# Performance work log

Hardware: AMD Instinct MI355X
Metric: run time of the kernel (lower is better)

The kernel has to match this reference:

```python
import jax, jax.numpy as jnp
import numpy as np

N_NODES = 100000
N_EDGES = 1600000
F_IN = 512
HIDDEN = 64
N_CLASS = 16


def spmm(edge_src, edge_dst, edge_val, dense):
    # sparse [N,N] @ dense [N,D] via gather-scale-scatter
    gathered = dense[edge_src] * edge_val[:, None]          # [E, D]
    return jax.ops.segment_sum(gathered, edge_dst, num_segments=N_NODES)


def setup_inputs() -> dict:
    key = jax.random.key(0)
    ks = jax.random.split(key, 8)
    return {
        "x": jax.random.normal(ks[0], (N_NODES, F_IN), dtype=jnp.float32),
        "edge_src": jax.random.randint(ks[1], (N_EDGES,), 0, N_NODES, dtype=jnp.int32),
        "edge_dst": jax.random.randint(ks[2], (N_EDGES,), 0, N_NODES, dtype=jnp.int32),
        "edge_val": jax.random.uniform(ks[3], (N_EDGES,), dtype=jnp.float32),
        "W1": jax.random.normal(ks[4], (F_IN, HIDDEN), dtype=jnp.float32) * (1.0 / np.sqrt(HIDDEN)),
        "b1": jax.random.normal(ks[5], (HIDDEN,), dtype=jnp.float32) * 0.01,
        "W2": jax.random.normal(ks[6], (HIDDEN, N_CLASS), dtype=jnp.float32) * (1.0 / np.sqrt(N_CLASS)),
        "b2": jax.random.normal(ks[7], (N_CLASS,), dtype=jnp.float32) * 0.01,
    }


def reference(x, edge_src, edge_dst, edge_val, W1, b1, W2, b2):
    # Layer 1: support = x @ W1 ; out = A @ support + b1 ; relu
    h = spmm(edge_src, edge_dst, edge_val, x @ W1) + b1      # [N, 64]
    h = jax.nn.relu(h)
    # dropout with training=False is identity (eval forward)
    # Layer 2
    logits = spmm(edge_src, edge_dst, edge_val, h @ W2) + b2  # [N, C]
    return jax.nn.softmax(logits, axis=1)
```

## Files before the change

### kernel.cpp

```cpp
#include <hip/hip_runtime.h>
#include <hip/hip_bf16.h>

#define N_NODES 100000
#define N_EDGES 1600000
#define F_IN    512
#define HID     64
#define NCLS    16

#define BSH     9
#define SCAN_NB 196
#define BM      128
#define BK      128
#define PA_EPB  4096
#define PA_NB   ((N_EDGES + PA_EPB - 1) / PA_EPB)
#define PREP_NB 128
#define GEMM_NB ((N_NODES + BM - 1) / BM)

typedef __attribute__((ext_vector_type(8))) short short8;
typedef __attribute__((ext_vector_type(4))) float f32x4;
typedef unsigned int u32;
typedef unsigned short u16;

__device__ inline void gload_lds16(const float* g, float* l) {
    __builtin_amdgcn_global_load_lds(
        (const __attribute__((address_space(1))) u32*)g,
        (__attribute__((address_space(3))) u32*)l, 16, 0, 0);
}

__device__ inline void split_bf16(float a, unsigned short& hi, unsigned short& lo) {
    unsigned u = __float_as_uint(a);
    hi = (unsigned short)(u >> 16);
    float hif = __uint_as_float(((unsigned)hi) << 16);
    float lof = a - hif;
    lo = (unsigned short)(__float_as_uint(lof) >> 16);
}

__device__ inline void split8(f32x4 a, f32x4 b, short8& hi, short8& lo) {
    #pragma unroll
    for (int i = 0; i < 4; i++) {
        u16 h, l;
        split_bf16(a[i], h, l);
        hi[i] = (short)h; lo[i] = (short)l;
    }
    #pragma unroll
    for (int i = 0; i < 4; i++) {
        u16 h, l;
        split_bf16(b[i], h, l);
        hi[4 + i] = (short)h; lo[4 + i] = (short)l;
    }
}

__global__ __launch_bounds__(256) void bhist_prep(const int* __restrict__ edst,
                                                  int* __restrict__ bh,
                                                  const float* __restrict__ W1,
                                                  unsigned short* __restrict__ Wg) {
    int tid = threadIdx.x;
    if (blockIdx.x >= PA_NB) {
        int idx = (blockIdx.x - PA_NB) * 256 + tid;
        if (idx < F_IN * HID) {
            int k = idx >> 6, n = idx & 63;
            unsigned short hi, lo;
            split_bf16(W1[idx], hi, lo);
            int nt = n >> 4, kc = k >> 5;
            int l  = ((k >> 3) & 3) * 16 + (n & 15);
            int j  = k & 7;
            long base = ((((long)nt * 16 + kc) * 2) * 64 + l) * 8 + j;
            Wg[base]       = hi;
            Wg[base + 512] = lo;
        }
        return;
    }
    __shared__ int hist[SCAN_NB];
    int e00 = blockIdx.x * PA_EPB;
    for (int i = tid; i < SCAN_NB; i += 256) hist[i] = 0;
    __syncthreads();
    #pragma unroll
    for (int j = 0; j < PA_EPB / 256; j++) {
        int e = e00 + j * 256 + tid;
        if (e < N_EDGES) atomicAdd(&hist[edst[e] >> BSH], 1);
    }
    __syncthreads();
    for (int i = tid; i < SCAN_NB; i += 256)
        bh[i * PA_NB + blockIdx.x] = hist[i];
}

__global__ __launch_bounds__(512) void colscan(int* __restrict__ bh,
                                               int* __restrict__ bsums) {
    __shared__ int sc[512];
    int t = threadIdx.x;
    int b = blockIdx.x;
    int v = (t < PA_NB) ? bh[b * PA_NB + t] : 0;
    sc[t] = v;
    __syncthreads();
    #pragma unroll
    for (int d = 1; d < 512; d <<= 1) {
        int u = (t >= d) ? sc[t - d] : 0;
        __syncthreads();
        sc[t] += u;
        __syncthreads();
    }
    if (t < PA_NB) bh[b * PA_NB + t] = sc[t] - v;
    if (t == 511) bsums[b] = sc[511];
}

__global__ __launch_bounds__(256) void scan_top(const int* __restrict__ bsums,
                                                int* __restrict__ bbase,
                                                int* __restrict__ off) {
    __shared__ int sc[256];
    int t = threadIdx.x;
    int v0 = (t < SCAN_NB) ? bsums[t] : 0;
    sc[t] = v0;
    __syncthreads();
    #pragma unroll
    for (int d = 1; d < 256; d <<= 1) {
        int v = (t >= d) ? sc[t - d] : 0;
        __syncthreads();
        sc[t] += v;
        __syncthreads();
    }
    bbase[t] = sc[t] - v0;
    if (t == 0) off[N_NODES] = N_EDGES;
}

__global__ __launch_bounds__(256, 2) void partA_gemm1(
        const int* __restrict__ esrc, const int* __restrict__ edst,
        const float* __restrict__ eval_, const int* __restrict__ bh,
        const int* __restrict__ bbase, int2* __restrict__ mid,
        const float* __restrict__ x, const unsigned short* __restrict__ Wg,
        float* __restrict__ support) {
    __shared__ float tile[BM * BK];
    __shared__ int   curs[SCAN_NB];

    const int tid = threadIdx.x;

    if (blockIdx.x < PA_NB) {
        int blk = blockIdx.x;
        int e00 = blk * PA_EPB;
        for (int i = tid; i < SCAN_NB; i += 256)
            curs[i] = bbase[i] + bh[i * PA_NB + blk];
        __syncthreads();
        #pragma unroll
        for (int j = 0; j < PA_EPB / 256; j++) {
            int e = e00 + j * 256 + tid;
            if (e < N_EDGES) {
                int d = edst[e];
                int b = d >> BSH;
                int pos = atomicAdd(&curs[b], 1);
                mid[pos] = make_int2(esrc[e] | ((d & 511) << 17),
                                     __float_as_int(eval_[e]));
            }
        }
        return;
    }

    const int l    = tid & 63;
    const int w    = tid >> 6;
    const int lr   = l & 15;
    const int lg   = l >> 4;
    const int row0 = (blockIdx.x - PA_NB) * BM;

    f32x4 acc[2][4] = {};

    for (int kb = 0; kb < F_IN; kb += BK) {
        #pragma unroll
        for (int j = 0; j < 16; j++) {
            int slotbase = j * 256 + w * 64;
            int slot     = slotbase + l;
            int row      = slot >> 5;
            int cl       = (slot & 31) ^ (row & 7);
            int rr       = row0 + row;
            if (rr > N_NODES - 1) rr = N_NODES - 1;
            gload_lds16(x + (long)rr * F_IN + kb + cl * 4, tile + slotbase * 4);
        }
        __syncthreads();

        #pragma unroll
        for (int ks = 0; ks < 4; ks++) {
            int kc = (kb >> 5) + ks;
            short8 ah[2], al[2];
            #pragma unroll
            for (int m = 0; m < 2; m++) {
                int r  = m * 64 + w * 16 + lr;
                int c0 = ks * 8 + lg * 2;
                f32x4 v0 = *(const f32x4*)&tile[r * BK + ((c0 ^ (r & 7)) << 2)];
                f32x4 v1 = *(const f32x4*)&tile[r * BK + (((c0 + 1) ^ (r & 7)) << 2)];
                split8(v0, v1, ah[m], al[m]);
            }
            #pragma unroll
            for (int nt = 0; nt < 4; nt++) {
                long bo = ((((long)nt * 16 + kc) * 2) * 64 + l) * 8;
                short8 bh8 = *(const short8*)(Wg + bo);
                short8 bl8 = *(const short8*)(Wg + bo + 512);
                #pragma unroll
                for (int m = 0; m < 2; m++) {
                    acc[m][nt] = __builtin_amdgcn_mfma_f32_16x16x32_bf16(ah[m], bh8, acc[m][nt], 0, 0, 0);
                    acc[m][nt] = __builtin_amdgcn_mfma_f32_16x16x32_bf16(ah[m], bl8, acc[m][nt], 0, 0, 0);
                    acc[m][nt] = __builtin_amdgcn_mfma_f32_16x16x32_bf16(al[m], bh8, acc[m][nt], 0, 0, 0);
                }
            }
        }
        __syncthreads();
    }

    #pragma unroll
    for (int m = 0; m < 2; m++) {
        #pragma unroll
        for (int nt = 0; nt < 4; nt++) {
            #pragma unroll
            for (int r = 0; r < 4; r++) {
                int row = row0 + m * 64 + w * 16 + lg * 4 + r;
                if (row < N_NODES)
                    support[(long)row * HID + nt * 16 + lr] = acc[m][nt][r];
            }
        }
    }
}

__global__ __launch_bounds__(512) void partB2(const int* __restrict__ bbase,
                                              const int* __restrict__ bsums,
                                              const int2* __restrict__ mid,
                                              int2* __restrict__ epk,
                                              int* __restrict__ off) {
    __shared__ int nh[512];
    __shared__ int sc[512];
    int t = threadIdx.x;
    int b = blockIdx.x;
    int start = bbase[b];
    int cntb  = bsums[b];

    nh[t] = 0;
    __syncthreads();

    for (int i = t; i < cntb; i += 512) {
        u32 ux = (u32)mid[start + i].x;
        atomicAdd(&nh[ux >> 17], 1);
    }
    __syncthreads();

    int c0 = nh[t];
    sc[t] = c0;
    __syncthreads();
    #pragma unroll
    for (int d = 1; d < 512; d <<= 1) {
        int u = (t >= d) ? sc[t - d] : 0;
        __syncthreads();
        sc[t] += u;
        __syncthreads();
    }
    int ex = start + sc[t] - c0;

    nh[t] = ex;
    int node = (b << BSH) + t;
    if (node < N_NODES) off[node] = ex;
    __syncthreads();

    for (int i = t; i < cntb; i += 512) {
        int2 m = mid[start + i];
        u32 ux = (u32)m.x;
        int pos = atomicAdd(&nh[ux >> 17], 1);
        epk[pos] = make_int2((int)(ux & 0x1FFFF), m.y);
    }
}

__global__ __launch_bounds__(256) void spmm1_fused(const int* __restrict__ off,
                                                   const int2* __restrict__ epk,
                                                   const float* __restrict__ sup,
                                                   const float* __restrict__ b1,
                                                   const float* __restrict__ W2,
                                                   float* __restrict__ sup2) {
    __shared__ float w2s[HID * NCLS];
    __shared__ float hrow[2][4][HID];
    int tid = threadIdx.x;
    for (int i = tid; i < HID * NCLS; i += 256) w2s[i] = W2[i];
    __syncthreads();

    int lane = tid & 63;
    int w    = tid >> 6;
    int c    = lane & 15, q = lane >> 4;
    float bl = b1[lane];

    for (int g = blockIdx.x; g < N_NODES / 4; g += gridDim.x) {
        int n = g * 4 + w;
        int e0 = off[n];
        int e1 = off[n + 1];
        float acc = 0.f;
        int e = e0;
        for (; e + 7 < e1; e += 8) {
            int2 p[8];
            float gg[8];
            #pragma unroll
            for (int j = 0; j < 8; j++) p[j] = epk[e + j];
            #pragma unroll
            for (int j = 0; j < 8; j++) gg[j] = sup[(long)p[j].x * HID + lane];
            #pragma unroll
            for (int j = 0; j < 8; j++) acc += __int_as_float(p[j].y) * gg[j];
        }
        for (; e + 3 < e1; e += 4) {
            int2 p0 = epk[e],     p1 = epk[e + 1];
            int2 p2 = epk[e + 2], p3 = epk[e + 3];
            float g0 = sup[(long)p0.x * HID + lane];
            float g1 = sup[(long)p1.x * HID + lane];
            float g2 = sup[(long)p2.x * HID + lane];
            float g3 = sup[(long)p3.x * HID + lane];
            acc += __int_as_float(p0.y) * g0 + __int_as_float(p1.y) * g1
                 + __int_as_float(p2.y) * g2 + __int_as_float(p3.y) * g3;
        }
        for (; e < e1; e++) {
            int2 p = epk[e];
            acc += __int_as_float(p.y) * sup[(long)p.x * HID + lane];
        }
        float hv = fmaxf(acc + bl, 0.f);

        int par = g & 1;
        hrow[par][w][lane] = hv;
        asm volatile("s_waitcnt lgkmcnt(0)" ::: "memory");
        __builtin_amdgcn_sched_barrier(0);

        float part = 0.f;
        #pragma unroll
        for (int k0 = 0; k0 < 16; k0++) {
            int k = q * 16 + k0;
            part += hrow[par][w][k] * w2s[k * NCLS + c];
        }
        part += __shfl_xor(part, 16);
        part += __shfl_xor(part, 32);
        if (lane < 16) sup2[(long)n * NCLS + c] = part;
    }
}

__global__ __launch_bounds__(256) void spmm2_softmax(const int* __restrict__ off,
                                                     const int2* __restrict__ epk,
                                                     const float* __restrict__ sup2,
                                                     const float* __restrict__ b2,
                                                     float* __restrict__ out) {
    int tid = threadIdx.x;
    int n   = blockIdx.x * 16 + (tid >> 4);
    int c   = tid & 15;
    if (n >= N_NODES) return;

    int e0 = off[n];
    int e1 = off[n + 1];
    float acc = 0.f;
    int e = e0;
    for (; e + 7 < e1; e += 8) {
        int2 p[8];
        float g[8];
        #pragma unroll
        for (int j = 0; j < 8; j++) p[j] = epk[e + j];
        #pragma unroll
        for (int j = 0; j < 8; j++) g[j] = sup2[(long)p[j].x * NCLS + c];
        #pragma unroll
        for (int j = 0; j < 8; j++) acc += __int_as_float(p[j].y) * g[j];
    }
    for (; e + 3 < e1; e += 4) {
        int2 p0 = epk[e],     p1 = epk[e + 1];
        int2 p2 = epk[e + 2], p3 = epk[e + 3];
        float g0 = sup2[(long)p0.x * NCLS + c];
        float g1 = sup2[(long)p1.x * NCLS + c];
        float g2 = sup2[(long)p2.x * NCLS + c];
        float g3 = sup2[(long)p3.x * NCLS + c];
        acc += __int_as_float(p0.y) * g0 + __int_as_float(p1.y) * g1
             + __int_as_float(p2.y) * g2 + __int_as_float(p3.y) * g3;
    }
    for (; e < e1; e++) {
        int2 p = epk[e];
        acc += __int_as_float(p.y) * sup2[(long)p.x * NCLS + c];
    }

    float lg = acc + b2[c];
    float m = lg;
    #pragma unroll
    for (int mask = 1; mask < 16; mask <<= 1)
        m = fmaxf(m, __shfl_xor(m, mask, 16));
    float p = expf(lg - m);
    float s = p;
    #pragma unroll
    for (int mask = 1; mask < 16; mask <<= 1)
        s += __shfl_xor(s, mask, 16);
    out[(long)n * NCLS + c] = p / s;
}

extern "C" void kernel_launch(void* const* d_in, const int* in_sizes, int n_in,
                              void* d_out, int out_size, void* d_ws, size_t ws_size,
                              hipStream_t stream) {
    const float* x     = (const float*)d_in[0];
    const int*   esrc  = (const int*)  d_in[1];
    const int*   edst  = (const int*)  d_in[2];
    const float* eval_ = (const float*)d_in[3];
    const float* W1    = (const float*)d_in[4];
    const float* b1    = (const float*)d_in[5];
    const float* W2    = (const float*)d_in[6];
    const float* b2    = (const float*)d_in[7];
    float* out = (float*)d_out;

    float* sup1  = (float*)d_ws;
    float* sup2  = sup1 + (long)N_NODES * HID;
    int2*  epk   = (int2*)(sup2 + (long)N_NODES * NCLS);
    int*   off   = (int*)(epk + N_EDGES);
    int*   bsums = off + 100004;
    int*   bbase = bsums + 256;
    int*   bh    = bbase + 256;
    unsigned short* Wg = (unsigned short*)(bh + 76640);
    int2*  mid   = (int2*)(Wg + 65536);

    bhist_prep<<<PA_NB + PREP_NB, 256, 0, stream>>>(edst, bh, W1, Wg);
    colscan<<<SCAN_NB, 512, 0, stream>>>(bh, bsums);
    scan_top<<<1,      256, 0, stream>>>(bsums, bbase, off);

    partA_gemm1<<<PA_NB + GEMM_NB, 256, 0, stream>>>(esrc, edst, eval_, bh,
                                                     bbase, mid, x, Wg, sup1);

    partB2<<<SCAN_NB, 512, 0, stream>>>(bbase, bsums, mid, epk, off);

    spmm1_fused<<<4096, 256, 0, stream>>>(off, epk, sup1, b1, W2, sup2);
    spmm2_softmax<<<(N_NODES + 15) / 16, 256, 0, stream>>>(off, epk, sup2, b2, out);
}
```

Measured before the change: 197.6 us.

## Fuse bucket-local CSR sort into partA/GEMM kernel using global done-counter spin-wait

Moves the second-pass bucket sort (partB2) into the partA+GEMM1 launch as extra trailing blocks. These blocks spin on a global counter until all partA scatter blocks have finished, then build per-node offsets and the packed edge list, with a 256-thread scan handling two nodes per thread. This removes one kernel launch and lets the sort overlap with the GEMM blocks. The cost is the spin-wait, which relies on the scatter blocks being scheduled before the waiting blocks to avoid deadlock, and the waiting blocks occupy CU slots.

```diff
diff --git a/kernel.cpp b/kernel.cpp
--- a/kernel.cpp
+++ b/kernel.cpp
@@ -105,7 +105,8 @@
 
 __global__ __launch_bounds__(256) void scan_top(const int* __restrict__ bsums,
                                                 int* __restrict__ bbase,
-                                                int* __restrict__ off) {
+                                                int* __restrict__ off,
+                                                int* __restrict__ done) {
     __shared__ int sc[256];
     int t = threadIdx.x;
     int v0 = (t < SCAN_NB) ? bsums[t] : 0;
@@ -119,13 +120,15 @@
         __syncthreads();
     }
     bbase[t] = sc[t] - v0;
-    if (t == 0) off[N_NODES] = N_EDGES;
-}
-
-__global__ __launch_bounds__(256, 2) void partA_gemm1(
+    if (t == 0) { off[N_NODES] = N_EDGES; *done = 0; }
+}
+
+__global__ __launch_bounds__(256, 2) void partAB_gemm1(
         const int* __restrict__ esrc, const int* __restrict__ edst,
         const float* __restrict__ eval_, const int* __restrict__ bh,
-        const int* __restrict__ bbase, int2* __restrict__ mid,
+        const int* __restrict__ bbase, const int* __restrict__ bsums,
+        int2* __restrict__ mid, int2* __restrict__ epk,
+        int* __restrict__ off, int* __restrict__ done,
         const float* __restrict__ x, const unsigned short* __restrict__ Wg,
         float* __restrict__ support) {
     __shared__ float tile[BM * BK];
@@ -149,6 +152,61 @@
                 mid[pos] = make_int2(esrc[e] | ((d & 511) << 17),
                                      __float_as_int(eval_[e]));
             }
+        }
+        __syncthreads();
+        __threadfence();
+        if (tid == 0) atomicAdd(done, 1);
+        return;
+    }
+
+    if (blockIdx.x >= PA_NB + GEMM_NB) {
+        int b = blockIdx.x - (PA_NB + GEMM_NB);
+        int start = bbase[b];
+        int cntb  = bsums[b];
+        int* nh = (int*)tile;
+        int* sc = ((int*)tile) + 512;
+
+        if (tid == 0) {
+            while (atomicAdd(done, 0) < PA_NB)
+                __builtin_amdgcn_s_sleep(8);
+        }
+        __syncthreads();
+        __threadfence();
+
+        nh[tid] = 0; nh[tid + 256] = 0;
+        __syncthreads();
+
+        for (int i = tid; i < cntb; i += 256) {
+            u32 ux = (u32)mid[start + i].x;
+            atomicAdd(&nh[ux >> 17], 1);
+        }
+        __syncthreads();
+
+        int c0 = nh[2 * tid], c1 = nh[2 * tid + 1];
+        int s = c0 + c1;
+        sc[tid] = s;
+        __syncthreads();
+        #pragma unroll
+        for (int d = 1; d < 256; d <<= 1) {
+            int u = (tid >= d) ? sc[tid - d] : 0;
+            __syncthreads();
+            sc[tid] += u;
+            __syncthreads();
+        }
+        int ex = start + sc[tid] - s;
+
+        nh[2 * tid]     = ex;
+        nh[2 * tid + 1] = ex + c0;
+        int node = (b << BSH) + 2 * tid;
+        if (node < N_NODES)     off[node]     = ex;
+        if (node + 1 < N_NODES) off[node + 1] = ex + c0;
+        __syncthreads();
+
+        for (int i = tid; i < cntb; i += 256) {
+            int2 m = mid[start + i];
+            u32 ux = (u32)m.x;
+            int pos = atomicAdd(&nh[ux >> 17], 1);
+            epk[pos] = make_int2((int)(ux & 0x1FFFF), m.y);
         }
         return;
     }
@@ -213,52 +271,6 @@
                     support[(long)row * HID + nt * 16 + lr] = acc[m][nt][r];
             }
         }
-    }
-}
-
-__global__ __launch_bounds__(512) void partB2(const int* __restrict__ bbase,
-                                              const int* __restrict__ bsums,
-                                              const int2* __restrict__ mid,
-                                              int2* __restrict__ epk,
-                                              int* __restrict__ off) {
-    __shared__ int nh[512];
-    __shared__ int sc[512];
-    int t = threadIdx.x;
-    int b = blockIdx.x;
-    int start = bbase[b];
-    int cntb  = bsums[b];
-
-    nh[t] = 0;
-    __syncthreads();
-
-    for (int i = t; i < cntb; i += 512) {
-        u32 ux = (u32)mid[start + i].x;
-        atomicAdd(&nh[ux >> 17], 1);
-    }
-    __syncthreads();
-
-    int c0 = nh[t];
-    sc[t] = c0;
-    __syncthreads();
-    #pragma unroll
-    for (int d = 1; d < 512; d <<= 1) {
-        int u = (t >= d) ? sc[t - d] : 0;
-        __syncthreads();
-        sc[t] += u;
-        __syncthreads();
-    }
-    int ex = start + sc[t] - c0;
-
-    nh[t] = ex;
-    int node = (b << BSH) + t;
-    if (node < N_NODES) off[node] = ex;
-    __syncthreads();
-
-    for (int i = t; i < cntb; i += 512) {
-        int2 m = mid[start + i];
-        u32 ux = (u32)m.x;
-        int pos = atomicAdd(&nh[ux >> 17], 1);
-        epk[pos] = make_int2((int)(ux & 0x1FFFF), m.y);
     }
 }
 
@@ -399,18 +411,17 @@
     int*   off   = (int*)(epk + N_EDGES);
     int*   bsums = off + 100004;
     int*   bbase = bsums + 256;
-    int*   bh    = bbase + 256;
+    int*   done  = bbase + 256;
+    int*   bh    = done + 16;
     unsigned short* Wg = (unsigned short*)(bh + 76640);
     int2*  mid   = (int2*)(Wg + 65536);
 
     bhist_prep<<<PA_NB + PREP_NB, 256, 0, stream>>>(edst, bh, W1, Wg);
     colscan<<<SCAN_NB, 512, 0, stream>>>(bh, bsums);
-    scan_top<<<1,      256, 0, stream>>>(bsums, bbase, off);
-
-    partA_gemm1<<<PA_NB + GEMM_NB, 256, 0, stream>>>(esrc, edst, eval_, bh,
-                                                     bbase, mid, x, Wg, sup1);
-
-    partB2<<<SCAN_NB, 512, 0, stream>>>(bbase, bsums, mid, epk, off);
+    scan_top<<<1,      256, 0, stream>>>(bsums, bbase, off, done);
+
+    partAB_gemm1<<<PA_NB + GEMM_NB + SCAN_NB, 256, 0, stream>>>(
+        esrc, edst, eval_, bh, bbase, bsums, mid, epk, off, done, x, Wg, sup1);
 
     spmm1_fused<<<4096, 256, 0, stream>>>(off, epk, sup1, b1, W2, sup2);
     spmm2_softmax<<<(N_NODES + 15) / 16, 256, 0, stream>>>(off, epk, sup2, b2, out);
```

After: 298.3 us. 51.0% more time.
